# Kernel optimization log

Hardware: AMD Instinct MI355X
Metric: run time of the kernel (lower is better)

## Reference

```python
import jax, jax.numpy as jnp
import numpy as np

BINS = 64

def _histc_rows(flat, bins):
    # flat: [N, L]; per-row torch.histc semantics with min=max=0 (use data min/max)
    lo = flat.min(axis=1, keepdims=True)
    hi = flat.max(axis=1, keepdims=True)
    same = hi == lo
    lo = jnp.where(same, lo - 1.0, lo)
    hi = jnp.where(same, hi + 1.0, hi)
    # bin index; value == hi maps to bins -> clipped into last bin (torch includes max)
    idx = jnp.floor((flat - lo) / (hi - lo) * bins).astype(jnp.int32)
    idx = jnp.clip(idx, 0, bins - 1)
    n = flat.shape[0]
    flat_idx = idx + (jnp.arange(n, dtype=jnp.int32)[:, None] * bins)
    hist = jnp.zeros((n * bins,), dtype=flat.dtype).at[flat_idx.ravel()].add(1.0)
    return hist.reshape(n, bins)

def reference(x, conv_w, conv_b, head_w, head_b):
    # Conv2d(1 -> C, k=3, valid), NCHW
    y = jax.lax.conv_general_dilated(
        x, conv_w, window_strides=(1, 1), padding='VALID',
        dimension_numbers=('NCHW', 'OIHW', 'NCHW'))
    y = y + conv_b[None, :, None, None]
    y = jax.nn.relu(y)
    b, c, h, w = y.shape
    hist = _histc_rows(y.reshape(b * c, h * w), BINS)  # [B*C, bins]
    feat = hist.reshape(b, c * BINS)
    return feat @ head_w.T + head_b

def setup_inputs() -> dict:
    key = jax.random.key(0)
    k1, k2, k3, k4, k5 = jax.random.split(key, 5)
    C, K, F = 64, 3, 1000
    return {
        'x': jax.random.normal(k1, (64, 1, 256, 256), dtype=jnp.float32),
        'conv_w': jax.random.normal(k2, (C, 1, K, K), dtype=jnp.float32) * 0.1,
        'conv_b': jax.random.normal(k3, (C,), dtype=jnp.float32) * 0.1,
        'head_w': jax.random.normal(k4, (F, C * BINS), dtype=jnp.float32) * 0.02,
        'head_b': jax.random.normal(k5, (F,), dtype=jnp.float32) * 0.02,
    }
```

## Files before the change

kernel.cpp:

```cpp
#include <hip/hip_runtime.h>


typedef short bf16x8 __attribute__((ext_vector_type(8)));
typedef float f32x16 __attribute__((ext_vector_type(16)));
typedef float f32x2 __attribute__((ext_vector_type(2)));

#define TPITCH 35
#define F_OUT_ 1000
#define KDIM_ 4096

__device__ __forceinline__ unsigned f2bf(float f) {
    unsigned u = __float_as_uint(f);
    return (u + 0x7FFFu + ((u >> 16) & 1u)) >> 16;
}
__device__ __forceinline__ float bf2f(unsigned h) { return __uint_as_float(h << 16); }

union FragU { uint4 u; bf16x8 v; };

__global__ __launch_bounds__(512, 6) void conv_minmax_kernel(
    const float* __restrict__ x, const float* __restrict__ cw,
    const float* __restrict__ cb, float* __restrict__ featQ,
    float* __restrict__ mnbuf, float* __restrict__ mxbuf)
{
    __shared__ unsigned t32[256 * TPITCH];
    __shared__ float red[1024];

    const int tid = threadIdx.x;
    const int lane = tid & 63;
    const int w = __builtin_amdgcn_readfirstlane(tid >> 6);
    const int b = blockIdx.x;
    const int seg = blockIdx.y;
    const int mrow = lane & 31;
    const int kg = lane >> 5;
    const int r0 = seg * 32;
    const int vlim = min(32, 254 - r0);

    featQ[(seg * 64 + b) * 512 + tid] = 0.f;

    FragU bwh[2], bwl[2];
#pragma unroll
    for (int g = 0; g < 2; ++g) {
        int och = g * 32 + mrow;
        unsigned hh[8], ll[8];
#pragma unroll
        for (int j = 0; j < 8; ++j) {
            int k = kg * 8 + j, dr = k >> 2, dc = k & 3;
            float wv = (kg == 1 && j == 7) ? cb[och]
                     : ((dr < 3 && dc < 3) ? cw[och * 9 + dr * 3 + dc] : 0.f);
            unsigned h = f2bf(wv);
            hh[j] = h;
            ll[j] = f2bf(wv - bf2f(h));
        }
        bwh[g].u = make_uint4(hh[0] | (hh[1] << 16), hh[2] | (hh[3] << 16),
                              hh[4] | (hh[5] << 16), hh[6] | (hh[7] << 16));
        bwl[g].u = make_uint4(ll[0] | (ll[1] << 16), ll[2] | (ll[3] << 16),
                              ll[4] | (ll[5] << 16), ll[6] | (ll[7] << 16));
    }
    f32x16 zc;
#pragma unroll
    for (int r = 0; r < 16; ++r) zc[r] = 0.f;

    const float* xb = x + (size_t)b * 65536;
    for (int i = tid; i < TPITCH * 256; i += 512) {
        int lrow = i >> 8, col = i & 255;
        int grow = r0 + lrow;
        float v = (grow < 256) ? xb[grow * 256 + col] : 0.f;
        unsigned h = f2bf(v);
        unsigned l = f2bf(v - bf2f(h));
        t32[col * TPITCH + lrow] = (l << 16) | h;
    }
    __syncthreads();

    f32x2 mn2A = {3.4e38f, 3.4e38f}, mx2A = {-3.4e38f, -3.4e38f};
    f32x2 mn2B = {3.4e38f, 3.4e38f}, mx2B = {-3.4e38f, -3.4e38f};
    const int cbase = w * 32;
    const int cend = min(cbase + 32, 254);
    const unsigned* tb = t32 + mrow + 2 * kg;
    unsigned a0 = tb[cbase * TPITCH],       r1a = tb[cbase * TPITCH + 1];
    unsigned a1 = tb[(cbase + 1) * TPITCH], r1b = tb[(cbase + 1) * TPITCH + 1];
#pragma unroll 2
    for (int c = cbase; c < cend; ++c) {
        unsigned a2 = tb[(c + 2) * TPITCH];
        unsigned r1c = tb[(c + 2) * TPITCH + 1];
        FragU ah, al;
        ah.u = make_uint4(__builtin_amdgcn_perm(a1, a0, 0x05040100u), a2,
                          __builtin_amdgcn_perm(r1b, r1a, 0x05040100u),
                          (r1c & 0xFFFFu) | 0x3F800000u);
        al.u = make_uint4(__builtin_amdgcn_perm(a1, a0, 0x07060302u), a2 >> 16,
                          __builtin_amdgcn_perm(r1b, r1a, 0x07060302u), r1c >> 16);
        a0 = a1; a1 = a2; r1a = r1b; r1b = r1c;
        f32x16 accA = __builtin_amdgcn_mfma_f32_32x32x16_bf16(ah.v, bwh[0].v, zc, 0, 0, 0);
        f32x16 accB = __builtin_amdgcn_mfma_f32_32x32x16_bf16(ah.v, bwh[1].v, zc, 0, 0, 0);
        accA = __builtin_amdgcn_mfma_f32_32x32x16_bf16(al.v, bwh[0].v, accA, 0, 0, 0);
        accB = __builtin_amdgcn_mfma_f32_32x32x16_bf16(al.v, bwh[1].v, accB, 0, 0, 0);
        accA = __builtin_amdgcn_mfma_f32_32x32x16_bf16(ah.v, bwl[0].v, accA, 0, 0, 0);
        accB = __builtin_amdgcn_mfma_f32_32x32x16_bf16(ah.v, bwl[1].v, accB, 0, 0, 0);
        if (vlim >= 32) {
#pragma unroll
            for (int r = 0; r < 16; r += 2) {
                f32x2 vA = {accA[r], accA[r + 1]}, vB = {accB[r], accB[r + 1]};
                mn2A = __builtin_elementwise_min(mn2A, vA);
                mx2A = __builtin_elementwise_max(mx2A, vA);
                mn2B = __builtin_elementwise_min(mn2B, vB);
                mx2B = __builtin_elementwise_max(mx2B, vB);
            }
        } else {
#pragma unroll
            for (int r = 0; r < 16; ++r) {
                int crow = (r & 3) + 8 * (r >> 2) + 4 * kg;
                float vA = (crow < vlim) ? accA[r] : accA[0];
                float vB = (crow < vlim) ? accB[r] : accB[0];
                mn2A[0] = fminf(mn2A[0], vA); mx2A[0] = fmaxf(mx2A[0], vA);
                mn2B[0] = fminf(mn2B[0], vB); mx2B[0] = fmaxf(mx2B[0], vB);
            }
        }
    }

    float mnA = fminf(mn2A[0], mn2A[1]), mxA = fmaxf(mx2A[0], mx2A[1]);
    float mnB = fminf(mn2B[0], mn2B[1]), mxB = fmaxf(mx2B[0], mx2B[1]);
    mnA = fminf(mnA, __shfl_xor(mnA, 32, 64));
    mxA = fmaxf(mxA, __shfl_xor(mxA, 32, 64));
    mnB = fminf(mnB, __shfl_xor(mnB, 32, 64));
    mxB = fmaxf(mxB, __shfl_xor(mxB, 32, 64));
    __syncthreads();
    if (lane < 32) {
        red[w * 64 + mrow] = mnA;        red[512 + w * 64 + mrow] = mxA;
        red[w * 64 + 32 + mrow] = mnB;   red[512 + w * 64 + 32 + mrow] = mxB;
    }
    __syncthreads();
    if (tid < 64) {
        float a = red[tid], c = red[512 + tid];
#pragma unroll
        for (int i = 1; i < 8; ++i) {
            a = fminf(a, red[i * 64 + tid]);
            c = fmaxf(c, red[512 + i * 64 + tid]);
        }
        mnbuf[((b * 64 + tid) << 3) | seg] = a;
        mxbuf[((b * 64 + tid) << 3) | seg] = c;
    }
}

__global__ __launch_bounds__(512, 6) void conv_hist_kernel(
    const float* __restrict__ x, const float* __restrict__ cw,
    const float* __restrict__ cb, float* __restrict__ featQ,
    const float* __restrict__ mnbuf, const float* __restrict__ mxbuf)
{
    __shared__ unsigned t32[256 * TPITCH];
    __shared__ unsigned hist[64 * 65];

    const int tid = threadIdx.x;
    const int lane = tid & 63;
    const int w = __builtin_amdgcn_readfirstlane(tid >> 6);
    const int b = blockIdx.x;
    const int seg = blockIdx.y;
    const int mrow = lane & 31;
    const int kg = lane >> 5;
    const int r0 = seg * 32;
    const int vlim = min(32, 254 - r0);

    float scg[2], nlsg[2];
#pragma unroll
    for (int g = 0; g < 2; ++g) {
        int och = g * 32 + mrow;
        float rmn = 3.402823466e38f, rmx = -3.402823466e38f;
#pragma unroll
        for (int s = 0; s < 8; ++s) {
            rmn = fminf(rmn, mnbuf[((b * 64 + och) << 3) | s]);
            rmx = fmaxf(rmx, mxbuf[((b * 64 + och) << 3) | s]);
        }
        float lo = fmaxf(rmn, 0.f);
        float hi = fmaxf(rmx, 0.f);
        if (hi == lo) { lo -= 1.f; hi += 1.f; }
        scg[g] = 64.f / (hi - lo);
        nlsg[g] = -lo * scg[g];
    }
    for (int i = tid; i < 64 * 65; i += 512) hist[i] = 0u;

    FragU bwh[2], bwl[2];
#pragma unroll
    for (int g = 0; g < 2; ++g) {
        int och = g * 32 + mrow;
        unsigned hh[8], ll[8];
#pragma unroll
        for (int j = 0; j < 8; ++j) {
            int k = kg * 8 + j, dr = k >> 2, dc = k & 3;
            float wv = (kg == 1 && j == 7) ? fmaf(cb[och], scg[g], nlsg[g])
                     : ((dr < 3 && dc < 3) ? cw[och * 9 + dr * 3 + dc] * scg[g] : 0.f);
            unsigned h = f2bf(wv);
            hh[j] = h;
            ll[j] = f2bf(wv - bf2f(h));
        }
        bwh[g].u = make_uint4(hh[0] | (hh[1] << 16), hh[2] | (hh[3] << 16),
                              hh[4] | (hh[5] << 16), hh[6] | (hh[7] << 16));
        bwl[g].u = make_uint4(ll[0] | (ll[1] << 16), ll[2] | (ll[3] << 16),
                              ll[4] | (ll[5] << 16), ll[6] | (ll[7] << 16));
    }
    f32x16 zc;
#pragma unroll
    for (int r = 0; r < 16; ++r) zc[r] = 0.f;

    const float* xb = x + (size_t)b * 65536;
    for (int i = tid; i < TPITCH * 256; i += 512) {
        int lrow = i >> 8, col = i & 255;
        int grow = r0 + lrow;
        float v = (grow < 256) ? xb[grow * 256 + col] : 0.f;
        unsigned h = f2bf(v);
        unsigned l = f2bf(v - bf2f(h));
        t32[col * TPITCH + lrow] = (l << 16) | h;
    }
    __syncthreads();

    const int cbase = w * 32;
    const int cend = min(cbase + 32, 254);
    unsigned* hA = hist + mrow * 65;
    unsigned* hB = hist + (32 + mrow) * 65;
    const unsigned* tb = t32 + mrow + 2 * kg;
    unsigned a0 = tb[cbase * TPITCH],       r1a = tb[cbase * TPITCH + 1];
    unsigned a1 = tb[(cbase + 1) * TPITCH], r1b = tb[(cbase + 1) * TPITCH + 1];
#pragma unroll 2
    for (int c = cbase; c < cend; ++c) {
        unsigned a2 = tb[(c + 2) * TPITCH];
        unsigned r1c = tb[(c + 2) * TPITCH + 1];
        FragU ah, al;
        ah.u = make_uint4(__builtin_amdgcn_perm(a1, a0, 0x05040100u), a2,
                          __builtin_amdgcn_perm(r1b, r1a, 0x05040100u),
                          (r1c & 0xFFFFu) | 0x3F800000u);
        al.u = make_uint4(__builtin_amdgcn_perm(a1, a0, 0x07060302u), a2 >> 16,
                          __builtin_amdgcn_perm(r1b, r1a, 0x07060302u), r1c >> 16);
        a0 = a1; a1 = a2; r1a = r1b; r1b = r1c;
        f32x16 accA = __builtin_amdgcn_mfma_f32_32x32x16_bf16(ah.v, bwh[0].v, zc, 0, 0, 0);
        f32x16 accB = __builtin_amdgcn_mfma_f32_32x32x16_bf16(ah.v, bwh[1].v, zc, 0, 0, 0);
        accA = __builtin_amdgcn_mfma_f32_32x32x16_bf16(al.v, bwh[0].v, accA, 0, 0, 0);
        accB = __builtin_amdgcn_mfma_f32_32x32x16_bf16(al.v, bwh[1].v, accB, 0, 0, 0);
        accA = __builtin_amdgcn_mfma_f32_32x32x16_bf16(ah.v, bwl[0].v, accA, 0, 0, 0);
        accB = __builtin_amdgcn_mfma_f32_32x32x16_bf16(ah.v, bwl[1].v, accB, 0, 0, 0);
        const f32x2 z2 = {0.f, 0.f}, c2 = {63.f, 63.f};
        if (vlim >= 32) {
#pragma unroll
            for (int r = 0; r < 16; r += 2) {
                f32x2 tA = __builtin_elementwise_min(
                    __builtin_elementwise_max((f32x2){accA[r], accA[r + 1]}, z2), c2);
                f32x2 tB = __builtin_elementwise_min(
                    __builtin_elementwise_max((f32x2){accB[r], accB[r + 1]}, z2), c2);
                atomicAdd(&hA[(int)tA[0]], 1u);
                atomicAdd(&hA[(int)tA[1]], 1u);
                atomicAdd(&hB[(int)tB[0]], 1u);
                atomicAdd(&hB[(int)tB[1]], 1u);
            }
        } else {
#pragma unroll
            for (int r = 0; r < 16; ++r) {
                int crow = (r & 3) + 8 * (r >> 2) + 4 * kg;
                float tA = fminf(fmaxf(accA[r], 0.f), 63.f);
                float tB = fminf(fmaxf(accB[r], 0.f), 63.f);
                int bA = (crow < vlim) ? (int)tA : 64;
                int bB = (crow < vlim) ? (int)tB : 64;
                atomicAdd(&hA[bA], 1u);
                atomicAdd(&hB[bB], 1u);
            }
        }
    }
    __syncthreads();

    for (int i = tid; i < 4096; i += 512) {
        int och = i >> 6, bin = i & 63;
        float cnt = (float)hist[och * 65 + bin];
        int k = (och << 6) | bin;
        atomicAdd(&featQ[((k >> 2) << 8) | (b << 2) | (k & 3)], cnt);
    }
}

__global__ __launch_bounds__(512) void head_kernel(
    const float* __restrict__ featQ, const float* __restrict__ hw,
    const float* __restrict__ hb, float* __restrict__ out)
{
    __shared__ float red[8][8][64];
    const int tid = threadIdx.x;
    const int m = tid & 63;
    const int kh = __builtin_amdgcn_readfirstlane(tid >> 6);
    const int n0 = blockIdx.x * 8;
    const float* fb = featQ + kh * 128 * 256 + (m << 2);
    const float* wp[8];
#pragma unroll
    for (int c = 0; c < 8; ++c)
        wp[c] = hw + (size_t)(n0 + c) * KDIM_ + kh * 512;

    float a[8] = {0.f, 0.f, 0.f, 0.f, 0.f, 0.f, 0.f, 0.f};
#pragma unroll 2
    for (int kq = 0; kq < 128; ++kq) {
        float4 f = *(const float4*)(fb + (kq << 8));
#pragma unroll
        for (int c = 0; c < 8; ++c) {
            float4 u = *(const float4*)(wp[c] + (kq << 2));
            a[c] += f.x * u.x + f.y * u.y + f.z * u.z + f.w * u.w;
        }
    }
#pragma unroll
    for (int c = 0; c < 8; ++c) red[kh][c][m] = a[c];
    __syncthreads();
    {
        int c = tid >> 6, mm = tid & 63;
        float v = hb[n0 + c];
#pragma unroll
        for (int q = 0; q < 8; ++q) v += red[q][c][mm];
        out[(size_t)mm * F_OUT_ + n0 + c] = v;
    }
}

extern "C" void kernel_launch(void* const* d_in, const int* in_sizes, int n_in,
                              void* d_out, int out_size, void* d_ws, size_t ws_size,
                              hipStream_t stream) {
    const float* x      = (const float*)d_in[0];
    const float* conv_w = (const float*)d_in[1];
    const float* conv_b = (const float*)d_in[2];
    const float* head_w = (const float*)d_in[3];
    const float* head_b = (const float*)d_in[4];
    float* out   = (float*)d_out;
    float* featQ = (float*)d_ws;
    float* mnbuf = featQ + 262144;
    float* mxbuf = mnbuf + 32768;

    dim3 grid(64, 8);
    conv_minmax_kernel<<<grid, 512, 0, stream>>>(x, conv_w, conv_b, featQ, mnbuf, mxbuf);
    conv_hist_kernel<<<grid, 512, 0, stream>>>(x, conv_w, conv_b, featQ, mnbuf, mxbuf);
    head_kernel<<<125, 512, 0, stream>>>(featQ, head_w, head_b, out);
}
```

Baseline: 215.6 us.

## Split histogram kernel across channel halves and transpose shared histogram layout

The conv_hist kernel now launches with a third grid dimension of 2, so each block handles 32 output channels instead of 64. This halves the MFMA and atomic work per block, shrinks the shared histogram, and doubles the block count to raise occupancy and parallelism. The histogram layout changes from channel-major with pitch 65 to bin-major with stride 32, so lanes hitting the same bin land in different banks. In exchange, each block still stages the full input tile into LDS and rebuilds it, so input loading and bf16 split conversion are done twice.

Measured after the change: 204.5 us. 5.1% less time.

```diff
diff --git a/kernel.cpp b/kernel.cpp
--- a/kernel.cpp
+++ b/kernel.cpp
@@ -146,54 +146,49 @@
     const float* __restrict__ mnbuf, const float* __restrict__ mxbuf)
 {
     __shared__ unsigned t32[256 * TPITCH];
-    __shared__ unsigned hist[64 * 65];
+    __shared__ unsigned hist[65 * 32];
 
     const int tid = threadIdx.x;
     const int lane = tid & 63;
     const int w = __builtin_amdgcn_readfirstlane(tid >> 6);
     const int b = blockIdx.x;
     const int seg = blockIdx.y;
+    const int gz = blockIdx.z;
     const int mrow = lane & 31;
     const int kg = lane >> 5;
     const int r0 = seg * 32;
     const int vlim = min(32, 254 - r0);
-
-    float scg[2], nlsg[2];
-#pragma unroll
-    for (int g = 0; g < 2; ++g) {
-        int och = g * 32 + mrow;
-        float rmn = 3.402823466e38f, rmx = -3.402823466e38f;
-#pragma unroll
-        for (int s = 0; s < 8; ++s) {
-            rmn = fminf(rmn, mnbuf[((b * 64 + och) << 3) | s]);
-            rmx = fmaxf(rmx, mxbuf[((b * 64 + och) << 3) | s]);
-        }
-        float lo = fmaxf(rmn, 0.f);
-        float hi = fmaxf(rmx, 0.f);
-        if (hi == lo) { lo -= 1.f; hi += 1.f; }
-        scg[g] = 64.f / (hi - lo);
-        nlsg[g] = -lo * scg[g];
-    }
-    for (int i = tid; i < 64 * 65; i += 512) hist[i] = 0u;
-
-    FragU bwh[2], bwl[2];
-#pragma unroll
-    for (int g = 0; g < 2; ++g) {
-        int och = g * 32 + mrow;
+    const int och = gz * 32 + mrow;
+
+    float rmn = 3.402823466e38f, rmx = -3.402823466e38f;
+#pragma unroll
+    for (int s = 0; s < 8; ++s) {
+        rmn = fminf(rmn, mnbuf[((b * 64 + och) << 3) | s]);
+        rmx = fmaxf(rmx, mxbuf[((b * 64 + och) << 3) | s]);
+    }
+    float lo = fmaxf(rmn, 0.f);
+    float hi = fmaxf(rmx, 0.f);
+    if (hi == lo) { lo -= 1.f; hi += 1.f; }
+    const float sc = 64.f / (hi - lo);
+    const float nls = -lo * sc;
+    for (int i = tid; i < 65 * 32; i += 512) hist[i] = 0u;
+
+    FragU bwh, bwl;
+    {
         unsigned hh[8], ll[8];
 #pragma unroll
         for (int j = 0; j < 8; ++j) {
             int k = kg * 8 + j, dr = k >> 2, dc = k & 3;
-            float wv = (kg == 1 && j == 7) ? fmaf(cb[och], scg[g], nlsg[g])
-                     : ((dr < 3 && dc < 3) ? cw[och * 9 + dr * 3 + dc] * scg[g] : 0.f);
+            float wv = (kg == 1 && j == 7) ? fmaf(cb[och], sc, nls)
+                     : ((dr < 3 && dc < 3) ? cw[och * 9 + dr * 3 + dc] * sc : 0.f);
             unsigned h = f2bf(wv);
             hh[j] = h;
             ll[j] = f2bf(wv - bf2f(h));
         }
-        bwh[g].u = make_uint4(hh[0] | (hh[1] << 16), hh[2] | (hh[3] << 16),
-                              hh[4] | (hh[5] << 16), hh[6] | (hh[7] << 16));
-        bwl[g].u = make_uint4(ll[0] | (ll[1] << 16), ll[2] | (ll[3] << 16),
-                              ll[4] | (ll[5] << 16), ll[6] | (ll[7] << 16));
+        bwh.u = make_uint4(hh[0] | (hh[1] << 16), hh[2] | (hh[3] << 16),
+                           hh[4] | (hh[5] << 16), hh[6] | (hh[7] << 16));
+        bwl.u = make_uint4(ll[0] | (ll[1] << 16), ll[2] | (ll[3] << 16),
+                           ll[4] | (ll[5] << 16), ll[6] | (ll[7] << 16));
     }
     f32x16 zc;
 #pragma unroll
@@ -212,8 +207,7 @@
 
     const int cbase = w * 32;
     const int cend = min(cbase + 32, 254);
-    unsigned* hA = hist + mrow * 65;
-    unsigned* hB = hist + (32 + mrow) * 65;
+    unsigned* hrow = hist + mrow;
     const unsigned* tb = t32 + mrow + 2 * kg;
     unsigned a0 = tb[cbase * TPITCH],       r1a = tb[cbase * TPITCH + 1];
     unsigned a1 = tb[(cbase + 1) * TPITCH], r1b = tb[(cbase + 1) * TPITCH + 1];
@@ -228,44 +222,34 @@
         al.u = make_uint4(__builtin_amdgcn_perm(a1, a0, 0x07060302u), a2 >> 16,
                           __builtin_amdgcn_perm(r1b, r1a, 0x07060302u), r1c >> 16);
         a0 = a1; a1 = a2; r1a = r1b; r1b = r1c;
-        f32x16 accA = __builtin_amdgcn_mfma_f32_32x32x16_bf16(ah.v, bwh[0].v, zc, 0, 0, 0);
-        f32x16 accB = __builtin_amdgcn_mfma_f32_32x32x16_bf16(ah.v, bwh[1].v, zc, 0, 0, 0);
-        accA = __builtin_amdgcn_mfma_f32_32x32x16_bf16(al.v, bwh[0].v, accA, 0, 0, 0);
-        accB = __builtin_amdgcn_mfma_f32_32x32x16_bf16(al.v, bwh[1].v, accB, 0, 0, 0);
-        accA = __builtin_amdgcn_mfma_f32_32x32x16_bf16(ah.v, bwl[0].v, accA, 0, 0, 0);
-        accB = __builtin_amdgcn_mfma_f32_32x32x16_bf16(ah.v, bwl[1].v, accB, 0, 0, 0);
+        f32x16 acc = __builtin_amdgcn_mfma_f32_32x32x16_bf16(ah.v, bwh.v, zc, 0, 0, 0);
+        acc = __builtin_amdgcn_mfma_f32_32x32x16_bf16(al.v, bwh.v, acc, 0, 0, 0);
+        acc = __builtin_amdgcn_mfma_f32_32x32x16_bf16(ah.v, bwl.v, acc, 0, 0, 0);
         const f32x2 z2 = {0.f, 0.f}, c2 = {63.f, 63.f};
         if (vlim >= 32) {
 #pragma unroll
             for (int r = 0; r < 16; r += 2) {
-                f32x2 tA = __builtin_elementwise_min(
-                    __builtin_elementwise_max((f32x2){accA[r], accA[r + 1]}, z2), c2);
-                f32x2 tB = __builtin_elementwise_min(
-                    __builtin_elementwise_max((f32x2){accB[r], accB[r + 1]}, z2), c2);
-                atomicAdd(&hA[(int)tA[0]], 1u);
-                atomicAdd(&hA[(int)tA[1]], 1u);
-                atomicAdd(&hB[(int)tB[0]], 1u);
-                atomicAdd(&hB[(int)tB[1]], 1u);
+                f32x2 t = __builtin_elementwise_min(
+                    __builtin_elementwise_max((f32x2){acc[r], acc[r + 1]}, z2), c2);
+                atomicAdd(&hrow[(int)t[0] << 5], 1u);
+                atomicAdd(&hrow[(int)t[1] << 5], 1u);
             }
         } else {
 #pragma unroll
             for (int r = 0; r < 16; ++r) {
                 int crow = (r & 3) + 8 * (r >> 2) + 4 * kg;
-                float tA = fminf(fmaxf(accA[r], 0.f), 63.f);
-                float tB = fminf(fmaxf(accB[r], 0.f), 63.f);
-                int bA = (crow < vlim) ? (int)tA : 64;
-                int bB = (crow < vlim) ? (int)tB : 64;
-                atomicAdd(&hA[bA], 1u);
-                atomicAdd(&hB[bB], 1u);
+                float t = fminf(fmaxf(acc[r], 0.f), 63.f);
+                int bin = (crow < vlim) ? (int)t : 64;
+                atomicAdd(&hrow[bin << 5], 1u);
             }
         }
     }
     __syncthreads();
 
-    for (int i = tid; i < 4096; i += 512) {
-        int och = i >> 6, bin = i & 63;
-        float cnt = (float)hist[och * 65 + bin];
-        int k = (och << 6) | bin;
+    for (int i = tid; i < 2048; i += 512) {
+        int o = i >> 6, bin = i & 63;
+        float cnt = (float)hist[(bin << 5) + o];
+        int k = ((gz * 32 + o) << 6) | bin;
         atomicAdd(&featQ[((k >> 2) << 8) | (b << 2) | (k & 3)], cnt);
     }
 }
@@ -320,8 +304,9 @@
     float* mnbuf = featQ + 262144;
     float* mxbuf = mnbuf + 32768;
 
-    dim3 grid(64, 8);
-    conv_minmax_kernel<<<grid, 512, 0, stream>>>(x, conv_w, conv_b, featQ, mnbuf, mxbuf);
-    conv_hist_kernel<<<grid, 512, 0, stream>>>(x, conv_w, conv_b, featQ, mnbuf, mxbuf);
+    dim3 g1(64, 8);
+    dim3 g2(64, 8, 2);
+    conv_minmax_kernel<<<g1, 512, 0, stream>>>(x, conv_w, conv_b, featQ, mnbuf, mxbuf);
+    conv_hist_kernel<<<g2, 512, 0, stream>>>(x, conv_w, conv_b, featQ, mnbuf, mxbuf);
     head_kernel<<<125, 512, 0, stream>>>(featQ, head_w, head_b, out);
 }
```
